# Kernel optimization log

Hardware: AMD Instinct MI355X
Metric: run time of the kernel (lower is better)

The kernel has to match this reference:

```python
import jax, jax.numpy as jnp
import numpy as np

B, N, G, H, A = 128, 49, 4096, 1024, 1024  # batch, regions, global feat dim, hidden, attn dim


def setup_inputs() -> dict:
    key = jax.random.key(0)
    ks = jax.random.split(key, 11)
    def w(k, shape, fan_in):
        return jax.random.normal(k, shape, jnp.float32) * (1.0 / np.sqrt(fan_in))
    return {
        "global_features": jax.random.normal(ks[0], (B, N, G), jnp.float32),
        "s_t": jax.random.normal(ks[1], (B, H), jnp.float32),
        "cov_a": jax.random.uniform(ks[2], (B, N, 1), jnp.float32),
        "W_g": w(ks[3], (G, G), G),
        "b_g": jnp.zeros((G,), jnp.float32),
        "W_gs": w(ks[4], (G, H), G),
        "b_gs": jnp.zeros((H,), jnp.float32),
        "W_h": w(ks[5], (H, A), H),
        "W_s": w(ks[6], (H, A), H),
        "W_c": w(ks[7], (1, A), 1),
        "v": w(ks[8], (A,), A),
    }


def reference(global_features, s_t, cov_a, W_g, b_g, W_gs, b_gs, W_h, W_s, W_c, v):
    # g_star = Linear(G->G) -> Linear(G->H) applied to region features  [B,N,H]
    g1 = jnp.einsum('bng,gk->bnk', global_features, W_g) + b_g
    g_star = jnp.einsum('bng,gh->bnh', g1, W_gs) + b_gs
    # additive (Bahdanau) energies: e = tanh(W_h g* + W_s s_t + W_c cov)  [B,N,A]
    e = jnp.tanh(
        jnp.einsum('bnh,ha->bna', g_star, W_h)
        + (s_t @ W_s)[:, None, :]
        + cov_a @ W_c
    )
    scores = jnp.einsum('bna,a->bn', e, v)          # [B,N]
    alpha = jax.nn.softmax(scores, axis=-1)          # attention over regions
    c_img = jnp.einsum('bn,bnh->bh', alpha, g_star)  # weighted sum context [B,H]
    return c_img
```

## Files before the change

### kernel.cpp

```cpp
#include <hip/hip_runtime.h>
#include <cstdint>
#include <cstddef>

typedef __bf16 bf16;
typedef __bf16 bf16x8 __attribute__((ext_vector_type(8)));
typedef __bf16 bf16v4 __attribute__((ext_vector_type(4)));
typedef float  f32x4  __attribute__((ext_vector_type(4)));

#define PB   128
#define PN   49
#define PG   4096
#define PH   1024
#define PA   1024
#define PM1  (PB * PN)

__global__ __launch_bounds__(256) void detect_kernel(
    const unsigned short* __restrict__ raw, int* __restrict__ flag)
{
    __shared__ int cnt;
    if (threadIdx.x == 0) cnt = 0;
    __syncthreads();
    unsigned short u = raw[threadIdx.x];
    float x = __uint_as_float(((unsigned int)u) << 16);
    float a = fabsf(x);
    atomicAdd(&cnt, (a >= 1e-7f && a <= 128.f) ? 1 : 0);
    __syncthreads();
    if (threadIdx.x == 0) flag[0] = (cnt >= 200) ? 1 : 0;
}

__device__ __forceinline__ float ldin(const void* p, size_t i, bool in32) {
    return in32 ? ((const float*)p)[i] : (float)((const bf16*)p)[i];
}

__device__ __forceinline__ void ldx8(const void* x, size_t k0, bool in32, float* xv) {
    if (in32) {
        f32x4 lo = *(const f32x4*)((const float*)x + k0);
        f32x4 hi = *(const f32x4*)((const float*)x + k0 + 4);
#pragma unroll
        for (int j = 0; j < 4; ++j) { xv[j] = lo[j]; xv[4 + j] = hi[j]; }
    } else {
        bf16x8 v = *(const bf16x8*)((const bf16*)x + k0);
#pragma unroll
        for (int j = 0; j < 8; ++j) xv[j] = (float)v[j];
    }
}

__global__ __launch_bounds__(256) void cvt_kernel(
    const void* __restrict__ in, const int* __restrict__ flag,
    bf16* __restrict__ out)
{
    const bool in32 = (flag[0] == 0);
    size_t i = ((size_t)blockIdx.x * 256 + threadIdx.x) * 8;
    bf16x8 o;
    if (in32) {
        f32x4 lo = *(const f32x4*)((const float*)in + i);
        f32x4 hi = *(const f32x4*)((const float*)in + i + 4);
#pragma unroll
        for (int j = 0; j < 4; ++j) { o[j] = (bf16)lo[j]; o[4 + j] = (bf16)hi[j]; }
    } else {
        o = *(const bf16x8*)((const bf16*)in + i);
    }
    *(bf16x8*)(out + i) = o;
}

template <int BF16OUT, int AADAPT, int BTERMS>
__global__ __launch_bounds__(256, 2) void gemm_kernel(
    const void* __restrict__ Araw, const bf16* __restrict__ Bt0,
    const bf16* __restrict__ Bt1, const int* __restrict__ flag,
    float* __restrict__ Cf, bf16* __restrict__ Cb,
    int M, int N, int K, int kTilesPerSplit)
{
    __shared__ __align__(16) bf16 lds[(BTERMS == 2 ? 3 : 2) * 128 * 64];
    bf16* As  = lds;
    bf16* Bs0 = lds + 128 * 64;
    bf16* Bs1 = lds + 2 * 128 * 64;

    const bool a32 = AADAPT && (flag[0] == 0);

    const int gx = gridDim.x, gy = gridDim.y;
    const int nwg = gx * gy * (int)gridDim.z;
    int flat = blockIdx.x + gx * (blockIdx.y + gy * blockIdx.z);
    {
        const int q8 = nwg >> 3, r8 = nwg & 7;
        const int xcd = flat & 7, sub = flat >> 3;
        flat = (xcd < r8 ? xcd * (q8 + 1) : r8 * (q8 + 1) + (xcd - r8) * q8) + sub;
    }
    const int bx  = flat % gx;
    const int byz = flat / gx;
    const int by  = byz % gy;
    const int bz  = byz / gy;

    const int tid  = threadIdx.x;
    const int m0   = by * 128;
    const int n0   = bx * 128;
    const int kt0  = bz * kTilesPerSplit;

    const int wave = tid >> 6;
    const int lane = tid & 63;
    const int wm   = (wave >> 1) * 64;
    const int wn   = (wave & 1) * 64;
    const int lm   = lane & 15;
    const int q    = lane >> 4;

    f32x4 acc[4][4];
#pragma unroll
    for (int i = 0; i < 4; ++i)
#pragma unroll
        for (int j = 0; j < 4; ++j) acc[i][j] = (f32x4)0.0f;

    for (int kt = 0; kt < kTilesPerSplit; ++kt) {
        const int k0 = (kt0 + kt) * 64;
#pragma unroll
        for (int it = 0; it < 4; ++it) {
            int p   = it * 256 + tid;
            int row = p >> 3;
            int lc  = ((p & 7) - row) & 7;
            size_t offB = (size_t)(n0 + row) * K + k0 + lc * 8;
            __builtin_amdgcn_global_load_lds((void*)(Bt0 + offB), (void*)(Bs0 + p * 8), 16, 0, 0);
            if (BTERMS == 2)
                __builtin_amdgcn_global_load_lds((void*)(Bt1 + offB), (void*)(Bs1 + p * 8), 16, 0, 0);
            size_t offA = (size_t)(m0 + row) * K + k0 + lc * 8;
            if (AADAPT) {
                bf16x8 va;
                if (a32) {
                    const float* pf = (const float*)Araw + offA;
                    f32x4 lo = *(const f32x4*)pf, hi = *(const f32x4*)(pf + 4);
#pragma unroll
                    for (int j = 0; j < 4; ++j) { va[j] = (bf16)lo[j]; va[4 + j] = (bf16)hi[j]; }
                } else {
                    va = *(const bf16x8*)((const bf16*)Araw + offA);
                }
                *(bf16x8*)(As + p * 8) = va;
            } else {
                __builtin_amdgcn_global_load_lds((void*)((const bf16*)Araw + offA),
                                                 (void*)(As + p * 8), 16, 0, 0);
            }
        }
        __syncthreads();

#pragma unroll
        for (int s = 0; s < 2; ++s) {
            bf16x8 af[4], bf0[4], bf1[4];
            const int c = s * 4 + q;
#pragma unroll
            for (int mi = 0; mi < 4; ++mi) {
                int row  = wm + mi * 16 + lm;
                int slot = row * 8 + ((c + row) & 7);
                af[mi] = *(const bf16x8*)(As + slot * 8);
            }
#pragma unroll
            for (int ni = 0; ni < 4; ++ni) {
                int row  = wn + ni * 16 + lm;
                int slot = row * 8 + ((c + row) & 7);
                bf0[ni] = *(const bf16x8*)(Bs0 + slot * 8);
                if (BTERMS == 2) bf1[ni] = *(const bf16x8*)(Bs1 + slot * 8);
            }
#pragma unroll
            for (int mi = 0; mi < 4; ++mi)
#pragma unroll
                for (int ni = 0; ni < 4; ++ni) {
                    acc[mi][ni] = __builtin_amdgcn_mfma_f32_16x16x32_bf16(
                        af[mi], bf0[ni], acc[mi][ni], 0, 0, 0);
                    if (BTERMS == 2)
                        acc[mi][ni] = __builtin_amdgcn_mfma_f32_16x16x32_bf16(
                            af[mi], bf1[ni], acc[mi][ni], 0, 0, 0);
                }
        }
        __syncthreads();
    }

#pragma unroll
    for (int mi = 0; mi < 4; ++mi)
#pragma unroll
        for (int ni = 0; ni < 4; ++ni)
#pragma unroll
            for (int r = 0; r < 4; ++r) {
                int row = m0 + wm + mi * 16 + q * 4 + r;
                int col = n0 + wn + ni * 16 + lm;
                if (BF16OUT)
                    Cb[(size_t)bz * M * N + (size_t)row * N + col] = (bf16)acc[mi][ni][r];
                else
                    Cf[(size_t)bz * M * N + (size_t)row * N + col] = acc[mi][ni][r];
            }
}

__global__ __launch_bounds__(256) void transpose_kernel(
    const void* __restrict__ in, const int* __restrict__ flag, int inMode,
    bf16* __restrict__ out, int R, int C)
{
    __shared__ bf16 tile[64][65];
    const bool in32 = (inMode == 0) && (flag[0] == 0);
    const int r0 = blockIdx.y * 64, c0 = blockIdx.x * 64;
    const int tx = threadIdx.x & 15, ty = threadIdx.x >> 4;
#pragma unroll
    for (int it = 0; it < 4; ++it) {
        int r = it * 16 + ty;
        size_t base = (size_t)(r0 + r) * C + c0 + tx * 4;
        if (in32) {
            f32x4 v = *(const f32x4*)((const float*)in + base);
#pragma unroll
            for (int i = 0; i < 4; ++i) tile[r][tx * 4 + i] = (bf16)v[i];
        } else {
            bf16v4 v = *(const bf16v4*)((const bf16*)in + base);
#pragma unroll
            for (int i = 0; i < 4; ++i) tile[r][tx * 4 + i] = v[i];
        }
    }
    __syncthreads();
#pragma unroll
    for (int it = 0; it < 4; ++it) {
        int c = it * 16 + ty;
        bf16v4 v;
#pragma unroll
        for (int i = 0; i < 4; ++i) v[i] = tile[tx * 4 + i][c];
        *(bf16v4*)(out + (size_t)(c0 + c) * R + r0 + tx * 4) = v;
    }
}

template <int WRITEN>
__global__ __launch_bounds__(256) void transpose_red2_kernel(
    const bf16* __restrict__ in, bf16* __restrict__ outT,
    bf16* __restrict__ outN, int R, int C)
{
    __shared__ bf16 tile[64][65];
    const size_t plane = (size_t)R * C;
    const int r0 = blockIdx.y * 64, c0 = blockIdx.x * 64;
    const int tx = threadIdx.x & 15, ty = threadIdx.x >> 4;
#pragma unroll
    for (int it = 0; it < 4; ++it) {
        int r = it * 16 + ty;
        size_t base = (size_t)(r0 + r) * C + c0 + tx * 4;
        bf16v4 va = *(const bf16v4*)(in + base);
        bf16v4 vb = *(const bf16v4*)(in + plane + base);
        bf16v4 s4;
#pragma unroll
        for (int i = 0; i < 4; ++i) {
            s4[i] = (bf16)((float)va[i] + (float)vb[i]);
            tile[r][tx * 4 + i] = s4[i];
        }
        if (WRITEN) *(bf16v4*)(outN + base) = s4;
    }
    __syncthreads();
#pragma unroll
    for (int it = 0; it < 4; ++it) {
        int c = it * 16 + ty;
        bf16v4 v;
#pragma unroll
        for (int i = 0; i < 4; ++i) v[i] = tile[tx * 4 + i][c];
        *(bf16v4*)(outT + (size_t)(c0 + c) * R + r0 + tx * 4) = v;
    }
}

__global__ __launch_bounds__(256) void rowdot_kernel(
    const void* __restrict__ x, const bf16* __restrict__ Wt,
    const void* __restrict__ addv, const int* __restrict__ flag, int xMode,
    float* __restrict__ y, int K)
{
    const bool raw32 = (flag[0] == 0);
    const bool x32   = (xMode == 0) || raw32;
    const int wave = threadIdx.x >> 6, lane = threadIdx.x & 63;
    const int c = blockIdx.x * 4 + wave;
    float s = 0.f;
    for (int k0 = lane * 8; k0 < K; k0 += 512) {
        bf16x8 w = *(const bf16x8*)(Wt + (size_t)c * K + k0);
        float xv[8];
        ldx8(x, (size_t)k0, x32, xv);
#pragma unroll
        for (int j = 0; j < 8; ++j) s += xv[j] * (float)w[j];
    }
#pragma unroll
    for (int off = 32; off; off >>= 1) s += __shfl_down(s, off);
    if (lane == 0) {
        float a = addv ? ldin(addv, c, raw32) : 0.f;
        y[c] = s + a;
    }
}

__global__ __launch_bounds__(256) void scores_kernel(
    const bf16* __restrict__ tP, const float* __restrict__ sprojP,
    const float* __restrict__ tbias, const void* __restrict__ cov,
    const void* __restrict__ Wc, const void* __restrict__ v,
    const int* __restrict__ flag, float* __restrict__ sc)
{
    const bool in32 = (flag[0] == 0);
    const int n = blockIdx.x, b = blockIdx.y, tid = threadIdx.x;
    __shared__ float red[4];
    const size_t trow = (size_t)(b * PN + n) * PA;
    const float cv = ldin(cov, b * PN + n, in32);
    float s = 0.f;
#pragma unroll
    for (int i = 0; i < 4; ++i) {
        int a = tid + i * 256;
        float tv = 0.f;
#pragma unroll
        for (int p = 0; p < 4; ++p)
            tv += (float)tP[(size_t)p * ((size_t)PM1 * PA) + trow + a];
        float sp = 0.f;
#pragma unroll
        for (int p = 0; p < 4; ++p)
            sp += sprojP[(size_t)p * (PB * PA) + (size_t)b * PA + a];
        s += ldin(v, a, in32) * tanhf(tv + sp + tbias[a] + cv * ldin(Wc, a, in32));
    }
#pragma unroll
    for (int off = 32; off; off >>= 1) s += __shfl_down(s, off);
    if ((tid & 63) == 0) red[tid >> 6] = s;
    __syncthreads();
    if (tid == 0) sc[b * PN + n] = red[0] + red[1] + red[2] + red[3];
}

__global__ __launch_bounds__(256) void weighted_kernel(
    const float* __restrict__ sc, const bf16* __restrict__ GFb,
    bf16* __restrict__ whi, bf16* __restrict__ wlo)
{
    const int b = blockIdx.y;
    const int g0 = blockIdx.x * 2048 + threadIdx.x * 8;
    float e[PN];
    float mx = -1e30f;
    for (int n = 0; n < PN; ++n) mx = fmaxf(mx, sc[b * PN + n]);
    float sum = 0.f;
    for (int n = 0; n < PN; ++n) { e[n] = expf(sc[b * PN + n] - mx); sum += e[n]; }
    const float inv = 1.f / sum;
    float acc[8];
#pragma unroll
    for (int j = 0; j < 8; ++j) acc[j] = 0.f;
    for (int n = 0; n < PN; ++n) {
        float al = e[n] * inv;
        bf16x8 gv = *(const bf16x8*)(GFb + (size_t)(b * PN + n) * PG + g0);
#pragma unroll
        for (int j = 0; j < 8; ++j) acc[j] += al * (float)gv[j];
    }
    bf16x8 h, l;
#pragma unroll
    for (int j = 0; j < 8; ++j) {
        h[j] = (bf16)acc[j];
        l[j] = (bf16)(acc[j] - (float)h[j]);
    }
    *(bf16x8*)(whi + (size_t)b * PG + g0) = h;
    *(bf16x8*)(wlo + (size_t)b * PG + g0) = l;
}

__global__ __launch_bounds__(256) void final_kernel(
    const float* __restrict__ cTP, const float* __restrict__ cbias,
    const int* __restrict__ flag, void* __restrict__ out)
{
    int i = blockIdx.x * 256 + threadIdx.x;
    int b = i >> 10, h = i & 1023;
    float s = cbias[h];
#pragma unroll
    for (int z = 0; z < 32; ++z) s += cTP[(size_t)z * (PH * PB) + h * PB + b];
    if (flag[0]) ((bf16*)out)[i] = (bf16)s;
    else         ((float*)out)[i] = s;
}

extern "C" void kernel_launch(void* const* d_in, const int* in_sizes, int n_in,
                              void* d_out, int out_size, void* d_ws, size_t ws_size,
                              hipStream_t stream)
{
    const void* GF  = d_in[0];
    const void* s_t = d_in[1];
    const void* cov = d_in[2];
    const void* Wg  = d_in[3];
    const void* bg  = d_in[4];
    const void* Wgs = d_in[5];
    const void* bgs = d_in[6];
    const void* Wh  = d_in[7];
    const void* Ws  = d_in[8];
    const void* Wc  = d_in[9];
    const void* v   = d_in[10];
    (void)in_sizes; (void)n_in; (void)out_size; (void)ws_size;

    const size_t MB = 1u << 20;
    char* W = (char*)d_ws;
    bf16*  GFb    = (bf16*) (W + 0);
    int*   flag   = (int*)  (W + 52 * MB);
    float* tbias  = (float*)(W + 52 * MB + 4096);
    float* cbias  = (float*)(W + 52 * MB + 8192);
    float* sc     = (float*)(W + 52 * MB + 12288);
    bf16*  s_tb   = (bf16*) (W + 52 * MB + 262144);
    bf16*  WsT    = (bf16*) (W + 53 * MB);
    bf16*  WhT    = (bf16*) (W + 55 * MB);
    float* sprojP = (float*)(W + 55 * MB);
    bf16*  WgsT   = (bf16*) (W + 58 * MB);
    bf16*  Wgb    = (bf16*) (W + 67 * MB);
    bf16*  WchT   = (bf16*) (W + 67 * MB);
    bf16*  tPb    = (bf16*) (W + 76 * MB);
    bf16*  wsum_hi= (bf16*) (W + 76 * MB);
    bf16*  wsum_lo= (bf16*) (W + 77 * MB);
    bf16*  WggsS  = (bf16*) (W + 101 * MB);
    bf16*  Wggs   = (bf16*) (W + 118 * MB);
    bf16*  WggsT  = (bf16*) (W + 127 * MB);
    float* cTP    = (float*)(W + 0);

    dim3 blk(256);

    detect_kernel<<<dim3(1), blk, 0, stream>>>((const unsigned short*)GF, flag);

    cvt_kernel<<<dim3((PM1 * PG) / 2048), blk, 0, stream>>>(GF, flag, GFb);
    cvt_kernel<<<dim3((PB * PH) / 2048), blk, 0, stream>>>(s_t, flag, s_tb);
    cvt_kernel<<<dim3((PG * PG) / 2048), blk, 0, stream>>>(Wg, flag, Wgb);
    transpose_kernel<<<dim3(PH / 64, PG / 64), blk, 0, stream>>>(Wgs, flag, 0, WgsT, PG, PH);
    transpose_kernel<<<dim3(PA / 64, PH / 64), blk, 0, stream>>>(Wh, flag, 0, WhT, PH, PA);
    transpose_kernel<<<dim3(PA / 64, PH / 64), blk, 0, stream>>>(Ws, flag, 0, WsT, PH, PA);

    rowdot_kernel<<<dim3(PH / 4), blk, 0, stream>>>(bg, WgsT, bgs, flag, 1, cbias, PG);
    rowdot_kernel<<<dim3(PA / 4), blk, 0, stream>>>(cbias, WhT, nullptr, flag, 0, tbias, PH);

    gemm_kernel<1, 0, 1><<<dim3(PH / 128, PG / 128, 2), blk, 0, stream>>>(
        Wgb, WgsT, nullptr, flag, nullptr, WggsS, PG, PH, PG, (PG / 64) / 2);
    transpose_red2_kernel<1><<<dim3(PH / 64, PG / 64), blk, 0, stream>>>(
        WggsS, WggsT, Wggs, PG, PH);

    gemm_kernel<1, 0, 1><<<dim3(PA / 128, PG / 128, 2), blk, 0, stream>>>(
        Wggs, WhT, nullptr, flag, nullptr, WggsS, PG, PA, PH, (PH / 64) / 2);
    transpose_red2_kernel<0><<<dim3(PA / 64, PG / 64), blk, 0, stream>>>(
        WggsS, WchT, nullptr, PG, PA);

    gemm_kernel<1, 0, 1><<<dim3(PA / 128, PM1 / 128, 4), blk, 0, stream>>>(
        GFb, WchT, nullptr, flag, nullptr, tPb, PM1, PA, PG, (PG / 64) / 4);

    gemm_kernel<0, 0, 1><<<dim3(PA / 128, 1, 4), blk, 0, stream>>>(
        s_tb, WsT, nullptr, flag, sprojP, nullptr, PB, PA, PH, (PH / 64) / 4);

    scores_kernel<<<dim3(PN, PB), blk, 0, stream>>>(tPb, sprojP, tbias, cov, Wc, v, flag, sc);
    weighted_kernel<<<dim3(PG / 2048, PB), blk, 0, stream>>>(sc, GFb, wsum_hi, wsum_lo);

    gemm_kernel<0, 0, 2><<<dim3(1, PH / 128, 32), blk, 0, stream>>>(
        WggsT, wsum_hi, wsum_lo, flag, cTP, nullptr, PH, PB, PG, (PG / 64) / 32);

    final_kernel<<<dim3((PB * PA) / 256), blk, 0, stream>>>(cTP, cbias, flag, d_out);
}
```

Before: 466.0 us.

## Materialize g_star via fused Wg·Wgs product and compute context directly

```diff
diff --git a/kernel.cpp b/kernel.cpp
--- a/kernel.cpp
+++ b/kernel.cpp
@@ -47,33 +47,34 @@
 
 __global__ __launch_bounds__(256) void cvt_kernel(
     const void* __restrict__ in, const int* __restrict__ flag,
-    bf16* __restrict__ out)
+    bf16* __restrict__ out, size_t total)
 {
     const bool in32 = (flag[0] == 0);
-    size_t i = ((size_t)blockIdx.x * 256 + threadIdx.x) * 8;
-    bf16x8 o;
-    if (in32) {
-        f32x4 lo = *(const f32x4*)((const float*)in + i);
-        f32x4 hi = *(const f32x4*)((const float*)in + i + 4);
-#pragma unroll
-        for (int j = 0; j < 4; ++j) { o[j] = (bf16)lo[j]; o[4 + j] = (bf16)hi[j]; }
-    } else {
-        o = *(const bf16x8*)((const bf16*)in + i);
-    }
-    *(bf16x8*)(out + i) = o;
-}
-
-template <int BF16OUT, int AADAPT, int BTERMS>
+    const size_t stride = (size_t)gridDim.x * 256 * 8;
+    for (size_t i = ((size_t)blockIdx.x * 256 + threadIdx.x) * 8; i < total; i += stride) {
+        bf16x8 o;
+        if (in32) {
+            f32x4 lo = *(const f32x4*)((const float*)in + i);
+            f32x4 hi = *(const f32x4*)((const float*)in + i + 4);
+#pragma unroll
+            for (int j = 0; j < 4; ++j) { o[j] = (bf16)lo[j]; o[4 + j] = (bf16)hi[j]; }
+        } else {
+            o = *(const bf16x8*)((const bf16*)in + i);
+        }
+        *(bf16x8*)(out + i) = o;
+    }
+}
+
+template <int BF16OUT, int AADAPT>
 __global__ __launch_bounds__(256, 2) void gemm_kernel(
     const void* __restrict__ Araw, const bf16* __restrict__ Bt0,
-    const bf16* __restrict__ Bt1, const int* __restrict__ flag,
+    const int* __restrict__ flag,
     float* __restrict__ Cf, bf16* __restrict__ Cb,
     int M, int N, int K, int kTilesPerSplit)
 {
-    __shared__ __align__(16) bf16 lds[(BTERMS == 2 ? 3 : 2) * 128 * 64];
+    __shared__ __align__(16) bf16 lds[2 * 128 * 64];
     bf16* As  = lds;
     bf16* Bs0 = lds + 128 * 64;
-    bf16* Bs1 = lds + 2 * 128 * 64;
 
     const bool a32 = AADAPT && (flag[0] == 0);
 
@@ -117,8 +118,6 @@
             int lc  = ((p & 7) - row) & 7;
             size_t offB = (size_t)(n0 + row) * K + k0 + lc * 8;
             __builtin_amdgcn_global_load_lds((void*)(Bt0 + offB), (void*)(Bs0 + p * 8), 16, 0, 0);
-            if (BTERMS == 2)
-                __builtin_amdgcn_global_load_lds((void*)(Bt1 + offB), (void*)(Bs1 + p * 8), 16, 0, 0);
             size_t offA = (size_t)(m0 + row) * K + k0 + lc * 8;
             if (AADAPT) {
                 bf16x8 va;
@@ -140,7 +139,7 @@
 
 #pragma unroll
         for (int s = 0; s < 2; ++s) {
-            bf16x8 af[4], bf0[4], bf1[4];
+            bf16x8 af[4], bf0[4];
             const int c = s * 4 + q;
 #pragma unroll
             for (int mi = 0; mi < 4; ++mi) {
@@ -153,18 +152,13 @@
                 int row  = wn + ni * 16 + lm;
                 int slot = row * 8 + ((c + row) & 7);
                 bf0[ni] = *(const bf16x8*)(Bs0 + slot * 8);
-                if (BTERMS == 2) bf1[ni] = *(const bf16x8*)(Bs1 + slot * 8);
             }
 #pragma unroll
             for (int mi = 0; mi < 4; ++mi)
 #pragma unroll
-                for (int ni = 0; ni < 4; ++ni) {
+                for (int ni = 0; ni < 4; ++ni)
                     acc[mi][ni] = __builtin_amdgcn_mfma_f32_16x16x32_bf16(
                         af[mi], bf0[ni], acc[mi][ni], 0, 0, 0);
-                    if (BTERMS == 2)
-                        acc[mi][ni] = __builtin_amdgcn_mfma_f32_16x16x32_bf16(
-                            af[mi], bf1[ni], acc[mi][ni], 0, 0, 0);
-                }
         }
         __syncthreads();
     }
@@ -185,11 +179,11 @@
 }
 
 __global__ __launch_bounds__(256) void transpose_kernel(
-    const void* __restrict__ in, const int* __restrict__ flag, int inMode,
+    const void* __restrict__ in, const int* __restrict__ flag,
     bf16* __restrict__ out, int R, int C)
 {
     __shared__ bf16 tile[64][65];
-    const bool in32 = (inMode == 0) && (flag[0] == 0);
+    const bool in32 = (flag[0] == 0);
     const int r0 = blockIdx.y * 64, c0 = blockIdx.x * 64;
     const int tx = threadIdx.x & 15, ty = threadIdx.x >> 4;
 #pragma unroll
@@ -217,10 +211,9 @@
     }
 }
 
-template <int WRITEN>
-__global__ __launch_bounds__(256) void transpose_red2_kernel(
-    const bf16* __restrict__ in, bf16* __restrict__ outT,
-    bf16* __restrict__ outN, int R, int C)
+template <int PLANES>
+__global__ __launch_bounds__(256) void transpose_red_kernel(
+    const bf16* __restrict__ in, bf16* __restrict__ outT, int R, int C)
 {
     __shared__ bf16 tile[64][65];
     const size_t plane = (size_t)R * C;
@@ -230,15 +223,15 @@
     for (int it = 0; it < 4; ++it) {
         int r = it * 16 + ty;
         size_t base = (size_t)(r0 + r) * C + c0 + tx * 4;
-        bf16v4 va = *(const bf16v4*)(in + base);
-        bf16v4 vb = *(const bf16v4*)(in + plane + base);
-        bf16v4 s4;
-#pragma unroll
-        for (int i = 0; i < 4; ++i) {
-            s4[i] = (bf16)((float)va[i] + (float)vb[i]);
-            tile[r][tx * 4 + i] = s4[i];
+        float s[4] = {0.f, 0.f, 0.f, 0.f};
+#pragma unroll
+        for (int p = 0; p < PLANES; ++p) {
+            bf16v4 v = *(const bf16v4*)(in + p * plane + base);
+#pragma unroll
+            for (int i = 0; i < 4; ++i) s[i] += (float)v[i];
         }
-        if (WRITEN) *(bf16v4*)(outN + base) = s4;
+#pragma unroll
+        for (int i = 0; i < 4; ++i) tile[r][tx * 4 + i] = (bf16)s[i];
     }
     __syncthreads();
 #pragma unroll
@@ -249,6 +242,23 @@
         for (int i = 0; i < 4; ++i) v[i] = tile[tx * 4 + i][c];
         *(bf16v4*)(outT + (size_t)(c0 + c) * R + r0 + tx * 4) = v;
     }
+}
+
+__global__ __launch_bounds__(256) void reduce4_kernel(
+    const bf16* __restrict__ in, bf16* __restrict__ out, size_t n)
+{
+    size_t i = ((size_t)blockIdx.x * 256 + threadIdx.x) * 8;
+    float s[8] = {0,0,0,0,0,0,0,0};
+#pragma unroll
+    for (int p = 0; p < 4; ++p) {
+        bf16x8 v = *(const bf16x8*)(in + (size_t)p * n + i);
+#pragma unroll
+        for (int j = 0; j < 8; ++j) s[j] += (float)v[j];
+    }
+    bf16x8 o;
+#pragma unroll
+    for (int j = 0; j < 8; ++j) o[j] = (bf16)s[j];
+    *(bf16x8*)(out + i) = o;
 }
 
 __global__ __launch_bounds__(256) void rowdot_kernel(
@@ -293,7 +303,7 @@
         int a = tid + i * 256;
         float tv = 0.f;
 #pragma unroll
-        for (int p = 0; p < 4; ++p)
+        for (int p = 0; p < 2; ++p)
             tv += (float)tP[(size_t)p * ((size_t)PM1 * PA) + trow + a];
         float sp = 0.f;
 #pragma unroll
@@ -308,48 +318,38 @@
     if (tid == 0) sc[b * PN + n] = red[0] + red[1] + red[2] + red[3];
 }
 
-__global__ __launch_bounds__(256) void weighted_kernel(
-    const float* __restrict__ sc, const bf16* __restrict__ GFb,
-    bf16* __restrict__ whi, bf16* __restrict__ wlo)
-{
-    const int b = blockIdx.y;
-    const int g0 = blockIdx.x * 2048 + threadIdx.x * 8;
+__global__ __launch_bounds__(256) void context_kernel(
+    const float* __restrict__ sc, const bf16* __restrict__ gstar,
+    const float* __restrict__ cbias, const int* __restrict__ flag,
+    void* __restrict__ out)
+{
+    const int b = blockIdx.x, tid = threadIdx.x;
+    const int h = tid * 4;
     float e[PN];
     float mx = -1e30f;
     for (int n = 0; n < PN; ++n) mx = fmaxf(mx, sc[b * PN + n]);
     float sum = 0.f;
     for (int n = 0; n < PN; ++n) { e[n] = expf(sc[b * PN + n] - mx); sum += e[n]; }
     const float inv = 1.f / sum;
-    float acc[8];
-#pragma unroll
-    for (int j = 0; j < 8; ++j) acc[j] = 0.f;
+    f32x4 cb = *(const f32x4*)(cbias + h);
+    float acc[4] = {cb[0], cb[1], cb[2], cb[3]};
     for (int n = 0; n < PN; ++n) {
         float al = e[n] * inv;
-        bf16x8 gv = *(const bf16x8*)(GFb + (size_t)(b * PN + n) * PG + g0);
-#pragma unroll
-        for (int j = 0; j < 8; ++j) acc[j] += al * (float)gv[j];
-    }
-    bf16x8 h, l;
-#pragma unroll
-    for (int j = 0; j < 8; ++j) {
-        h[j] = (bf16)acc[j];
-        l[j] = (bf16)(acc[j] - (float)h[j]);
-    }
-    *(bf16x8*)(whi + (size_t)b * PG + g0) = h;
-    *(bf16x8*)(wlo + (size_t)b * PG + g0) = l;
-}
-
-__global__ __launch_bounds__(256) void final_kernel(
-    const float* __restrict__ cTP, const float* __restrict__ cbias,
-    const int* __restrict__ flag, void* __restrict__ out)
-{
-    int i = blockIdx.x * 256 + threadIdx.x;
-    int b = i >> 10, h = i & 1023;
-    float s = cbias[h];
-#pragma unroll
-    for (int z = 0; z < 32; ++z) s += cTP[(size_t)z * (PH * PB) + h * PB + b];
-    if (flag[0]) ((bf16*)out)[i] = (bf16)s;
-    else         ((float*)out)[i] = s;
+        bf16v4 g = *(const bf16v4*)(gstar + (size_t)(b * PN + n) * PH + h);
+#pragma unroll
+        for (int j = 0; j < 4; ++j) acc[j] += al * (float)g[j];
+    }
+    if (flag[0]) {
+        bf16v4 o;
+#pragma unroll
+        for (int j = 0; j < 4; ++j) o[j] = (bf16)acc[j];
+        *(bf16v4*)((bf16*)out + (size_t)b * PH + h) = o;
+    } else {
+        f32x4 o;
+#pragma unroll
+        for (int j = 0; j < 4; ++j) o[j] = acc[j];
+        *(f32x4*)((float*)out + (size_t)b * PH + h) = o;
+    }
 }
 
 extern "C" void kernel_launch(void* const* d_in, const int* in_sizes, int n_in,
@@ -372,6 +372,7 @@
     const size_t MB = 1u << 20;
     char* W = (char*)d_ws;
     bf16*  GFb    = (bf16*) (W + 0);
+    bf16*  g_star = (bf16*) (W + 0);
     int*   flag   = (int*)  (W + 52 * MB);
     float* tbias  = (float*)(W + 52 * MB + 4096);
     float* cbias  = (float*)(W + 52 * MB + 8192);
@@ -379,53 +380,44 @@
     bf16*  s_tb   = (bf16*) (W + 52 * MB + 262144);
     bf16*  WsT    = (bf16*) (W + 53 * MB);
     bf16*  WhT    = (bf16*) (W + 55 * MB);
-    float* sprojP = (float*)(W + 55 * MB);
-    bf16*  WgsT   = (bf16*) (W + 58 * MB);
-    bf16*  Wgb    = (bf16*) (W + 67 * MB);
-    bf16*  WchT   = (bf16*) (W + 67 * MB);
-    bf16*  tPb    = (bf16*) (W + 76 * MB);
-    bf16*  wsum_hi= (bf16*) (W + 76 * MB);
-    bf16*  wsum_lo= (bf16*) (W + 77 * MB);
-    bf16*  WggsS  = (bf16*) (W + 101 * MB);
-    bf16*  Wggs   = (bf16*) (W + 118 * MB);
-    bf16*  WggsT  = (bf16*) (W + 127 * MB);
-    float* cTP    = (float*)(W + 0);
+    float* sprojP = (float*)(W + 57 * MB);
+    bf16*  WgsT   = (bf16*) (W + 59 * MB);
+    bf16*  WggsT  = (bf16*) (W + 59 * MB);
+    bf16*  WggsS  = (bf16*) (W + 67 * MB);
+    bf16*  gP     = (bf16*) (W + 67 * MB);
+    bf16*  t2P    = (bf16*) (W + 67 * MB);
 
     dim3 blk(256);
 
     detect_kernel<<<dim3(1), blk, 0, stream>>>((const unsigned short*)GF, flag);
 
-    cvt_kernel<<<dim3((PM1 * PG) / 2048), blk, 0, stream>>>(GF, flag, GFb);
-    cvt_kernel<<<dim3((PB * PH) / 2048), blk, 0, stream>>>(s_t, flag, s_tb);
-    cvt_kernel<<<dim3((PG * PG) / 2048), blk, 0, stream>>>(Wg, flag, Wgb);
-    transpose_kernel<<<dim3(PH / 64, PG / 64), blk, 0, stream>>>(Wgs, flag, 0, WgsT, PG, PH);
-    transpose_kernel<<<dim3(PA / 64, PH / 64), blk, 0, stream>>>(Wh, flag, 0, WhT, PH, PA);
-    transpose_kernel<<<dim3(PA / 64, PH / 64), blk, 0, stream>>>(Ws, flag, 0, WsT, PH, PA);
+    cvt_kernel<<<dim3(2048), blk, 0, stream>>>(GF, flag, GFb, (size_t)PM1 * PG);
+    cvt_kernel<<<dim3(64), blk, 0, stream>>>(s_t, flag, s_tb, (size_t)PB * PH);
+    transpose_kernel<<<dim3(PH / 64, PG / 64), blk, 0, stream>>>(Wgs, flag, WgsT, PG, PH);
+    transpose_kernel<<<dim3(PA / 64, PH / 64), blk, 0, stream>>>(Wh, flag, WhT, PH, PA);
+    transpose_kernel<<<dim3(PA / 64, PH / 64), blk, 0, stream>>>(Ws, flag, WsT, PH, PA);
 
     rowdot_kernel<<<dim3(PH / 4), blk, 0, stream>>>(bg, WgsT, bgs, flag, 1, cbias, PG);
     rowdot_kernel<<<dim3(PA / 4), blk, 0, stream>>>(cbias, WhT, nullptr, flag, 0, tbias, PH);
 
-    gemm_kernel<1, 0, 1><<<dim3(PH / 128, PG / 128, 2), blk, 0, stream>>>(
-        Wgb, WgsT, nullptr, flag, nullptr, WggsS, PG, PH, PG, (PG / 64) / 2);
-    transpose_red2_kernel<1><<<dim3(PH / 64, PG / 64), blk, 0, stream>>>(
-        WggsS, WggsT, Wggs, PG, PH);
-
-    gemm_kernel<1, 0, 1><<<dim3(PA / 128, PG / 128, 2), blk, 0, stream>>>(
-        Wggs, WhT, nullptr, flag, nullptr, WggsS, PG, PA, PH, (PH / 64) / 2);
-    transpose_red2_kernel<0><<<dim3(PA / 64, PG / 64), blk, 0, stream>>>(
-        WggsS, WchT, nullptr, PG, PA);
-
-    gemm_kernel<1, 0, 1><<<dim3(PA / 128, PM1 / 128, 4), blk, 0, stream>>>(
-        GFb, WchT, nullptr, flag, nullptr, tPb, PM1, PA, PG, (PG / 64) / 4);
-
-    gemm_kernel<0, 0, 1><<<dim3(PA / 128, 1, 4), blk, 0, stream>>>(
-        s_tb, WsT, nullptr, flag, sprojP, nullptr, PB, PA, PH, (PH / 64) / 4);
-
-    scores_kernel<<<dim3(PN, PB), blk, 0, stream>>>(tPb, sprojP, tbias, cov, Wc, v, flag, sc);
-    weighted_kernel<<<dim3(PG / 2048, PB), blk, 0, stream>>>(sc, GFb, wsum_hi, wsum_lo);
-
-    gemm_kernel<0, 0, 2><<<dim3(1, PH / 128, 32), blk, 0, stream>>>(
-        WggsT, wsum_hi, wsum_lo, flag, cTP, nullptr, PH, PB, PG, (PG / 64) / 32);
-
-    final_kernel<<<dim3((PB * PA) / 256), blk, 0, stream>>>(cTP, cbias, flag, d_out);
-}
+    gemm_kernel<1, 1><<<dim3(PH / 128, PG / 128, 4), blk, 0, stream>>>(
+        Wg, WgsT, flag, nullptr, WggsS, PG, PH, PG, (PG / 64) / 4);
+    transpose_red_kernel<4><<<dim3(PH / 64, PG / 64), blk, 0, stream>>>(
+        WggsS, WggsT, PG, PH);
+
+    gemm_kernel<1, 0><<<dim3(PH / 128, PM1 / 128, 4), blk, 0, stream>>>(
+        GFb, WggsT, flag, nullptr, gP, PM1, PH, PG, (PG / 64) / 4);
+    reduce4_kernel<<<dim3((PM1 * PH) / 2048), blk, 0, stream>>>(
+        gP, g_star, (size_t)PM1 * PH);
+
+    gemm_kernel<1, 0><<<dim3(PA / 128, PM1 / 128, 2), blk, 0, stream>>>(
+        g_star, WhT, flag, nullptr, t2P, PM1, PA, PH, (PH / 64) / 2);
+
+    gemm_kernel<0, 0><<<dim3(PA / 128, 1, 4), blk, 0, stream>>>(
+        s_tb, WsT, flag, sprojP, nullptr, PB, PA, PH, (PH / 64) / 4);
+
+    scores_kernel<<<dim3(PN, PB), blk, 0, stream>>>(
+        t2P, sprojP, tbias, cov, Wc, v, flag, sc);
+
+    context_kernel<<<dim3(PB), blk, 0, stream>>>(sc, g_star, cbias, flag, d_out);
+}
```

After: 495.5 us. +6.3%, slower.
